# Kernel optimization log

Measured on AMD Instinct MI355X. Metric: run time of the kernel, lower is better.

Reference implementation:

```python
import jax, jax.numpy as jnp
import numpy as np

N = 100000
EPS = 1e-5

def gcn_conv(x, W, b, src, dst, n):
    # linear transform first (PyG GCNConv): [N, H]
    h = x @ W
    # add self-loops
    loop = jnp.arange(n, dtype=src.dtype)
    s = jnp.concatenate([src, loop])
    d = jnp.concatenate([dst, loop])
    # symmetric normalization deg^{-1/2}[s] * deg^{-1/2}[d]
    deg = jax.ops.segment_sum(jnp.ones_like(d, dtype=h.dtype), d, num_segments=n)
    dinv = jnp.where(deg > 0, jax.lax.rsqrt(jnp.maximum(deg, 1.0) * 0 + jnp.where(deg > 0, deg, 1.0)), 0.0)
    norm = dinv[s] * dinv[d]
    msg = h[s] * norm[:, None]          # gather + scale: [E+N, H]
    out = jax.ops.segment_sum(msg, d, num_segments=n)  # scatter-add
    return out + b

def batch_norm(x, gamma, beta):
    mu = jnp.mean(x, axis=0)
    var = jnp.mean((x - mu) ** 2, axis=0)  # biased var, as BatchNorm1d training
    return (x - mu) * jax.lax.rsqrt(var + EPS) * gamma + beta

def setup_inputs() -> dict:
    key = jax.random.key(0)
    ks = jax.random.split(key, 8)
    D, H, O = 64, 64, 32
    E = 1600000
    x = jax.random.normal(ks[0], (N, D), dtype=jnp.float32)
    edge_index = jax.random.randint(ks[1], (2, E), 0, N, dtype=jnp.int64)
    W1 = jax.random.normal(ks[2], (D, H), dtype=jnp.float32) / np.sqrt(D)
    b1 = jnp.zeros((H,), dtype=jnp.float32)
    W2 = jax.random.normal(ks[3], (H, H), dtype=jnp.float32) / np.sqrt(H)
    b2 = jnp.zeros((H,), dtype=jnp.float32)
    gamma1 = jnp.ones((H,), dtype=jnp.float32); beta1 = jnp.zeros((H,), dtype=jnp.float32)
    gamma2 = jnp.ones((H,), dtype=jnp.float32); beta2 = jnp.zeros((H,), dtype=jnp.float32)
    Wfc = jax.random.normal(ks[4], (H, O), dtype=jnp.float32) / np.sqrt(H)
    bfc = jnp.zeros((O,), dtype=jnp.float32)
    return {"x": x, "edge_index": edge_index, "W1": W1, "b1": b1, "gamma1": gamma1, "beta1": beta1,
            "W2": W2, "b2": b2, "gamma2": gamma2, "beta2": beta2, "Wfc": Wfc, "bfc": bfc}

def reference(x, edge_index, W1, b1, gamma1, beta1, W2, b2, gamma2, beta2, Wfc, bfc):
    src, dst = edge_index[0], edge_index[1]
    h = jax.nn.relu(gcn_conv(x, W1, b1, src, dst, N))
    h = batch_norm(h, gamma1, beta1)
    h = jax.nn.relu(gcn_conv(h, W2, b2, src, dst, N))
    h = batch_norm(h, gamma2, beta2)
    return h @ Wfc + bfc
```

## Files before the change

### kernel.cpp

```cpp
#include <hip/hip_runtime.h>
#include <hip/hip_bf16.h>
#include <cstdint>
#include <cstddef>

#define NS 8
#define SCHUNK 12500
#define BKB 512
#define SUBC 32

static __device__ __forceinline__ unsigned pack_bf16(float a, float b) {
  __hip_bfloat16 lo = __float2bfloat16(a), hi = __float2bfloat16(b);
  unsigned short ulo = *reinterpret_cast<unsigned short*>(&lo);
  unsigned short uhi = *reinterpret_cast<unsigned short*>(&hi);
  return ((unsigned)uhi << 16) | ulo;
}
static __device__ __forceinline__ float blo(unsigned u) {
  union { unsigned q; float f; } x; x.q = u << 16; return x.f;
}
static __device__ __forceinline__ float bhi(unsigned u) {
  union { unsigned q; float f; } x; x.q = u & 0xffff0000u; return x.f;
}


__launch_bounds__(256)
__global__ void bucket_kernel(const int* __restrict__ src, const int* __restrict__ dst,
                              int E, int cap, unsigned magic,
                              int* __restrict__ bcur,
                              int* __restrict__ bkt_d, int* __restrict__ bkt_s) {
  __shared__ int cnt8[NS], base8[NS], gbase8[NS], cur8[NS];
  __shared__ int stg_d[3200], stg_s[3200];
  int t = threadIdx.x;
  int chunk = (E + BKB - 1) / BKB;
  int ebeg = blockIdx.x * chunk;
  int eend = min(E, ebeg + chunk);
  int nloc = eend - ebeg;
  if (t < NS) { cnt8[t] = 0; cur8[t] = 0; }
  __syncthreads();

  int dl[13], sl[13]; unsigned cl[13];
  int nr = (nloc + 255) >> 8;
#pragma unroll 13
  for (int u = 0; u < nr; ++u) {
    int li = (u << 8) + t;
    bool v = li < nloc;
    int i = ebeg + (v ? li : 0);
    int d = v ? __builtin_nontemporal_load(&dst[i]) : 0;
    int s = v ? __builtin_nontemporal_load(&src[i]) : 0;
    unsigned sli = (unsigned)(((unsigned long long)(unsigned)d * magic) >> 45);
    dl[u] = d; sl[u] = s; cl[u] = sli;
    if (v) atomicAdd(&cnt8[sli], 1);
  }
  __syncthreads();
  if (t == 0) {
    int run = 0;
#pragma unroll
    for (int q = 0; q < NS; ++q) { base8[q] = run; run += cnt8[q]; }
  }
  __syncthreads();
  if (t < NS) gbase8[t] = atomicAdd(&bcur[t], cnt8[t]);
#pragma unroll 13
  for (int u = 0; u < nr; ++u) {
    int li = (u << 8) + t;
    if (li < nloc) {
      unsigned sli = cl[u];
      int pos = atomicAdd(&cur8[sli], 1) + base8[sli];
      stg_d[pos] = dl[u]; stg_s[pos] = sl[u];
    }
  }
  __syncthreads();
#pragma unroll
  for (int q = 0; q < NS; ++q) {
    int c = cnt8[q], b = base8[q], g = gbase8[q];
    int* od = bkt_d + (size_t)q * cap + g;
    int* os = bkt_s + (size_t)q * cap + g;
    for (int i = t; i < c; i += 256) { od[i] = stg_d[b + i]; os[i] = stg_s[b + i]; }
  }
}

__launch_bounds__(1024)
__global__ void count_b_kernel(const int* __restrict__ bkt_d, const int* __restrict__ bcur,
                               int cap, int n, int* __restrict__ partials) {
  __shared__ int hist[SCHUNK];
  int slice = blockIdx.x & (NS - 1), sub = blockIdx.x >> 3;
  int sbase = slice * SCHUNK;
  int bs = bcur[slice];
  const int* bk = bkt_d + (size_t)slice * cap;
  for (int l = threadIdx.x; l < SCHUNK; l += 1024) hist[l] = 0;
  __syncthreads();
  int beg = (int)((long long)sub * bs / SUBC);
  int end = (int)((long long)(sub + 1) * bs / SUBC);
  for (int i = beg + threadIdx.x; i < end; i += 1024)
    atomicAdd(&hist[bk[i] - sbase], 1);
  __syncthreads();
  for (int l = threadIdx.x; l < SCHUNK; l += 1024)
    partials[(size_t)sub * n + sbase + l] = hist[l];
}

__global__ void scan1_kernel(int* __restrict__ partials, int n, int* __restrict__ rowptr,
                             float* __restrict__ dinv, int* __restrict__ bsums) {
  __shared__ int sm[1024];
  int t = threadIdx.x;
  int gid = blockIdx.x * 1024 + t;
  int v = 0;
  if (gid < n) {
#pragma unroll
    for (int s = 0; s < SUBC; ++s) {
      int c = partials[(size_t)s * n + gid];
      partials[(size_t)s * n + gid] = v;
      v += c;
    }
    dinv[gid] = rsqrtf((float)(v + 1));
  }
  sm[t] = v;
  __syncthreads();
  for (int off = 1; off < 1024; off <<= 1) {
    int x = (t >= off) ? sm[t - off] : 0;
    __syncthreads();
    sm[t] += x;
    __syncthreads();
  }
  if (gid < n) rowptr[gid] = sm[t] - v;
  if (t == 1023) bsums[blockIdx.x] = sm[1023];
}

__global__ void scan2_kernel(int* __restrict__ bsums, int nb) {
  __shared__ int sm[1024];
  int t = threadIdx.x;
  int v = (t < nb) ? bsums[t] : 0;
  sm[t] = v;
  __syncthreads();
  for (int off = 1; off < 1024; off <<= 1) {
    int x = (t >= off) ? sm[t - off] : 0;
    __syncthreads();
    sm[t] += x;
    __syncthreads();
  }
  if (t < nb) bsums[t] = sm[t] - v;
}

__global__ void scan3_kernel(int n, int E, int* __restrict__ rowptr, const int* __restrict__ bsums) {
  int i = blockIdx.x * blockDim.x + threadIdx.x;
  if (i < n) rowptr[i] += bsums[i >> 10];
  if (i == 0) rowptr[n] = E;
}

__launch_bounds__(1024)
__global__ void scatter_b_kernel(const int* __restrict__ bkt_d, const int* __restrict__ bkt_s,
                                 const int* __restrict__ bcur, int cap, int n,
                                 const int* __restrict__ rowptr, const int* __restrict__ partials,
                                 int* __restrict__ adj) {
  __shared__ int base[SCHUNK];
  int slice = blockIdx.x & (NS - 1), sub = blockIdx.x >> 3;
  int sbase = slice * SCHUNK;
  int bs = bcur[slice];
  const int* bd = bkt_d + (size_t)slice * cap;
  const int* bsc = bkt_s + (size_t)slice * cap;
  const int* pref = partials + (size_t)sub * n;
  for (int l = threadIdx.x; l < SCHUNK; l += 1024)
    base[l] = rowptr[sbase + l] + pref[sbase + l];
  __syncthreads();
  int beg = (int)((long long)sub * bs / SUBC);
  int end = (int)((long long)(sub + 1) * bs / SUBC);
  for (int i = beg + threadIdx.x; i < end; i += 1024) {
    int d = bd[i], s = bsc[i];
    int pos = atomicAdd(&base[d - sbase], 1);
    adj[pos] = s;
  }
}


template <int OUT, bool BF16OUT, bool BN, bool ABF16>
__launch_bounds__(256)
__global__ void gemm_kernel(const void* __restrict__ Ap, const float* __restrict__ W,
                            const float* __restrict__ bnacc,
                            const float* __restrict__ gamma, const float* __restrict__ beta,
                            const float* __restrict__ bias, const float* __restrict__ rowscale,
                            void* __restrict__ Cout, int n, float invn) {
  constexpr int OQ = OUT / 4;
  __shared__ float lds[64 * 65];
  __shared__ float sc_s[64], sh_s[64];
  int t = threadIdx.x;
  int row0 = blockIdx.x * 64;
  int rows = n - row0; if (rows > 64) rows = 64;

  if (BN) {
    if (t < 64) {
      float su = 0.f, sq = 0.f;
#pragma unroll
      for (int c = 0; c < 8; ++c) {
        su += bnacc[c * 128 + t];
        sq += bnacc[c * 128 + 64 + t];
      }
      float mu = su * invn;
      float var = sq * invn - mu * mu;
      float sc = gamma[t] * rsqrtf(var + 1e-5f);
      sc_s[t] = sc;
      sh_s[t] = fmaf(-mu, sc, beta[t]);
    }
    __syncthreads();
  }

  if (ABF16) {
    const uint4* A4 = (const uint4*)((const unsigned short*)Ap + (size_t)row0 * 64);
#pragma unroll
    for (int j = 0; j < 2; ++j) {
      int idx = t + j * 256;
      int r = idx >> 3, c8 = idx & 7;
      uint4 v = make_uint4(0, 0, 0, 0);
      if (r < rows) v = A4[idx];
      float f[8] = {blo(v.x), bhi(v.x), blo(v.y), bhi(v.y),
                    blo(v.z), bhi(v.z), blo(v.w), bhi(v.w)};
      float* p = &lds[r * 65 + c8 * 8];
#pragma unroll
      for (int q = 0; q < 8; ++q) {
        float xv = f[q];
        if (BN) xv = fmaf(xv, sc_s[c8 * 8 + q], sh_s[c8 * 8 + q]);
        p[q] = xv;
      }
    }
  } else {
    const float4* A4 = (const float4*)((const float*)Ap + (size_t)row0 * 64);
#pragma unroll
    for (int j = 0; j < 4; ++j) {
      int idx = t + j * 256;
      int r = idx >> 4, c4 = idx & 15;
      float4 v = make_float4(0.f, 0.f, 0.f, 0.f);
      if (r < rows) v = A4[idx];
      if (BN) {
        int c = c4 * 4;
        v.x = fmaf(v.x, sc_s[c + 0], sh_s[c + 0]);
        v.y = fmaf(v.y, sc_s[c + 1], sh_s[c + 1]);
        v.z = fmaf(v.z, sc_s[c + 2], sh_s[c + 2]);
        v.w = fmaf(v.w, sc_s[c + 3], sh_s[c + 3]);
      }
      float* p = &lds[r * 65 + c4 * 4];
      p[0] = v.x; p[1] = v.y; p[2] = v.z; p[3] = v.w;
    }
  }
  __syncthreads();

  const int w = __builtin_amdgcn_readfirstlane(t >> 6);
  const int r = t & 63;
  float acc[OQ];
#pragma unroll
  for (int o = 0; o < OQ; ++o) acc[o] = 0.f;
  const float* Ar = &lds[r * 65];
  const float* Wp = W + w * OQ;
  for (int k = 0; k < 64; ++k) {
    float a = Ar[k];
#pragma unroll
    for (int o = 0; o < OQ; ++o) acc[o] = fmaf(a, Wp[k * OUT + o], acc[o]);
  }
  if (rowscale) {
    int rr = row0 + r; if (rr >= n) rr = n - 1;
    float rs = rowscale[rr];
#pragma unroll
    for (int o = 0; o < OQ; ++o) acc[o] *= rs;
  }
  if (bias) {
    const float* Bp = bias + w * OQ;
#pragma unroll
    for (int o = 0; o < OQ; ++o) acc[o] += Bp[o];
  }

  if (r < rows) {
    if (BF16OUT) {
      unsigned pk[OQ / 2];
#pragma unroll
      for (int o2 = 0; o2 < OQ / 2; ++o2) pk[o2] = pack_bf16(acc[2 * o2], acc[2 * o2 + 1]);
      uint4* cp = (uint4*)((__hip_bfloat16*)Cout + (size_t)(row0 + r) * OUT + w * OQ);
#pragma unroll
      for (int j = 0; j < OQ / 8; ++j) {
        uint4 v; v.x = pk[j * 4]; v.y = pk[j * 4 + 1]; v.z = pk[j * 4 + 2]; v.w = pk[j * 4 + 3];
        cp[j] = v;
      }
    } else {
      float4* cp = (float4*)((float*)Cout + (size_t)(row0 + r) * OUT + w * OQ);
#pragma unroll
      for (int j = 0; j < OQ / 4; ++j)
        cp[j] = make_float4(acc[j * 4], acc[j * 4 + 1], acc[j * 4 + 2], acc[j * 4 + 3]);
    }
  }
}


__launch_bounds__(256, 8)
__global__ void agg_kernel(const __hip_bfloat16* __restrict__ g, const int* __restrict__ rowptr,
                           const int* __restrict__ adj, const float* __restrict__ dinv,
                           const float* __restrict__ bias, __hip_bfloat16* __restrict__ out,
                           float* __restrict__ bnacc, int n) {
  const int tid = threadIdx.x;
  const int lane = tid & 63;
  const int wave = tid >> 6;
  const int grp = lane >> 3;
  const int sub = lane & 7;
  const int gw = blockIdx.x * 4 + wave;

  const unsigned short* gu = (const unsigned short*)g;

  int d = gw * 8 + grp;
  int beg = rowptr[d];
  int k = rowptr[d + 1] - beg;
  float di = dinv[d];

  const uint4 v0 = *(const uint4*)(gu + (((size_t)d) << 6) + sub * 8);
  float acc[8];
  acc[0] = blo(v0.x); acc[1] = bhi(v0.x);
  acc[2] = blo(v0.y); acc[3] = bhi(v0.y);
  acc[4] = blo(v0.z); acc[5] = bhi(v0.z);
  acc[6] = blo(v0.w); acc[7] = bhi(v0.w);

  int kmax = k;
  kmax = max(kmax, __shfl_xor(kmax, 8));
  kmax = max(kmax, __shfl_xor(kmax, 16));
  kmax = max(kmax, __shfl_xor(kmax, 32));

  for (int j0 = 0; j0 < kmax; j0 += 8) {
    uint4 vv[8];
    float w[8];
#pragma unroll
    for (int u = 0; u < 8; ++u) {
      int idx = j0 + u;
      int aoff = (idx < k) ? idx : 0;
      int s = __builtin_nontemporal_load(&adj[beg + aoff]);
      unsigned su = ((unsigned)s < (unsigned)n) ? (unsigned)s : (unsigned)d;
      vv[u] = *(const uint4*)(gu + (((size_t)su) << 6) + sub * 8);
      w[u] = (idx < k) ? 1.f : 0.f;
    }
#pragma unroll
    for (int u = 0; u < 8; ++u) {
      acc[0] = fmaf(w[u], blo(vv[u].x), acc[0]);
      acc[1] = fmaf(w[u], bhi(vv[u].x), acc[1]);
      acc[2] = fmaf(w[u], blo(vv[u].y), acc[2]);
      acc[3] = fmaf(w[u], bhi(vv[u].y), acc[3]);
      acc[4] = fmaf(w[u], blo(vv[u].z), acc[4]);
      acc[5] = fmaf(w[u], bhi(vv[u].z), acc[5]);
      acc[6] = fmaf(w[u], blo(vv[u].w), acc[6]);
      acc[7] = fmaf(w[u], bhi(vv[u].w), acc[7]);
    }
  }

  float bias8[8];
  {
    const float4* bp = (const float4*)(bias + sub * 8);
    float4 b0 = bp[0], b1 = bp[1];
    bias8[0]=b0.x; bias8[1]=b0.y; bias8[2]=b0.z; bias8[3]=b0.w;
    bias8[4]=b1.x; bias8[5]=b1.y; bias8[6]=b1.z; bias8[7]=b1.w;
  }

  float o[8], s1[8], s2[8];
#pragma unroll
  for (int j = 0; j < 8; ++j) {
    float v = fmaf(acc[j], di, bias8[j]);
    v = fmaxf(v, 0.f);
    o[j] = v;
    s1[j] = v;
    s2[j] = v * v;
  }
  uint4 ov;
  ov.x = pack_bf16(o[0], o[1]); ov.y = pack_bf16(o[2], o[3]);
  ov.z = pack_bf16(o[4], o[5]); ov.w = pack_bf16(o[6], o[7]);
  *(uint4*)((unsigned short*)out + (((size_t)d) << 6) + sub * 8) = ov;

#pragma unroll
  for (int j = 0; j < 8; ++j) {
    s1[j] += __shfl_xor(s1[j], 8);  s2[j] += __shfl_xor(s2[j], 8);
    s1[j] += __shfl_xor(s1[j], 16); s2[j] += __shfl_xor(s2[j], 16);
    s1[j] += __shfl_xor(s1[j], 32); s2[j] += __shfl_xor(s2[j], 32);
  }
  __shared__ float redA[4][64], redB[4][64];
  if (lane < 8) {
#pragma unroll
    for (int j = 0; j < 8; ++j) {
      redA[wave][sub * 8 + j] = s1[j];
      redB[wave][sub * 8 + j] = s2[j];
    }
  }
  __syncthreads();
  if (tid < 64) {
    float a = redA[0][tid] + redA[1][tid] + redA[2][tid] + redA[3][tid];
    float b = redB[0][tid] + redB[1][tid] + redB[2][tid] + redB[3][tid];
    float* dst = bnacc + (blockIdx.x & 7) * 128;
    atomicAdd(&dst[tid], a);
    atomicAdd(&dst[64 + tid], b);
  }
}


extern "C" void kernel_launch(void* const* d_in, const int* in_sizes, int n_in,
                              void* d_out, int out_size, void* d_ws, size_t ws_size,
                              hipStream_t stream) {
  const float* x      = (const float*)d_in[0];
  const int*   ei     = (const int*)d_in[1];
  const float* W1     = (const float*)d_in[2];
  const float* b1     = (const float*)d_in[3];
  const float* gamma1 = (const float*)d_in[4];
  const float* beta1  = (const float*)d_in[5];
  const float* W2     = (const float*)d_in[6];
  const float* b2     = (const float*)d_in[7];
  const float* gamma2 = (const float*)d_in[8];
  const float* beta2  = (const float*)d_in[9];
  const float* Wfc    = (const float*)d_in[10];
  const float* bfc    = (const float*)d_in[11];

  int n = in_sizes[0] / 64;
  int E = in_sizes[1] / 2;
  const int* src = ei;
  const int* dst = ei + E;

  char* base = (char*)d_ws;
  size_t off = 0;
  auto alloc = [&](size_t bytes) -> char* {
    char* p = base + off;
    off += (bytes + 255) & ~(size_t)255;
    return p;
  };
  int*   rowptr = (int*)alloc((size_t)(n + 1) * 4);
  int*   adj    = (int*)alloc(((size_t)E + 64) * 4);
  int*   bsums  = (int*)alloc(1024 * 4);
  float* dinv   = (float*)alloc((size_t)n * 4);
  float* bn     = (float*)alloc(2048 * 4);
  int*   bcur   = (int*)alloc(NS * 4);
  __hip_bfloat16* hbuf = (__hip_bfloat16*)alloc((size_t)n * 64 * 2);
  char*  rraw   = alloc((size_t)n * 64 * 4);
  __hip_bfloat16* rbuf = (__hip_bfloat16*)rraw;
  int cap = 210000;
  int* bkt_d = (int*)rraw;
  int* bkt_s = bkt_d + (size_t)NS * cap;
  int* partials = (int*)hbuf;
  (void)ws_size; (void)n_in; (void)out_size;

  hipMemsetAsync(bn, 0, 2048 * 4, stream);
  hipMemsetAsync(bcur, 0, NS * 4, stream);

  unsigned magic = (unsigned)(((1ULL << 45) + SCHUNK - 1) / SCHUNK);
  bucket_kernel<<<BKB, 256, 0, stream>>>(src, dst, E, cap, magic, bcur, bkt_d, bkt_s);
  count_b_kernel<<<NS * SUBC, 1024, 0, stream>>>(bkt_d, bcur, cap, n, partials);
  int nb = (n + 1023) / 1024;
  scan1_kernel<<<nb, 1024, 0, stream>>>(partials, n, rowptr, dinv, bsums);
  scan2_kernel<<<1, 1024, 0, stream>>>(bsums, nb);
  scan3_kernel<<<(n + 255) / 256, 256, 0, stream>>>(n, E, rowptr, bsums);
  scatter_b_kernel<<<NS * SUBC, 1024, 0, stream>>>(bkt_d, bkt_s, bcur, cap, n,
                                                   rowptr, partials, adj);

  int gg = (n + 63) / 64;
  int ga = n / 32;
  float invn = 1.0f / (float)n;
  gemm_kernel<64, true, false, false><<<gg, 256, 0, stream>>>(
      x, W1, nullptr, nullptr, nullptr, nullptr, dinv, hbuf, n, 0.f);
  agg_kernel<<<ga, 256, 0, stream>>>(hbuf, rowptr, adj, dinv, b1, rbuf, bn, n);
  gemm_kernel<64, true, true, true><<<gg, 256, 0, stream>>>(
      rbuf, W2, bn, gamma1, beta1, nullptr, dinv, hbuf, n, invn);
  agg_kernel<<<ga, 256, 0, stream>>>(hbuf, rowptr, adj, dinv, b2, rbuf, bn + 1024, n);
  gemm_kernel<32, false, true, true><<<gg, 256, 0, stream>>>(
      rbuf, Wfc, bn + 1024, gamma2, beta2, bfc, nullptr, d_out, n, invn);
}
```

Measured before the change: 271.6 us.

## Replace bucketed LDS CSR build with direct global atomic degree count and scatter

Replaces the multi-pass bucketing CSR construction (slice bucketing, per-slice shared-memory histograms, partial-count scans) with a direct global-atomic degree histogram and a global-atomic scatter into adjacency. This removes two passes over the bucket arrays and the 32-way partial prefix work. In exchange it relies on 1.6M global atomics per pass on random destinations, and the scatter writes to adj land at random addresses.

```diff
diff --git a/kernel.cpp b/kernel.cpp
--- a/kernel.cpp
+++ b/kernel.cpp
@@ -2,11 +2,6 @@
 #include <hip/hip_bf16.h>
 #include <cstdint>
 #include <cstddef>
-
-#define NS 8
-#define SCHUNK 12500
-#define BKB 512
-#define SUBC 32
 
 static __device__ __forceinline__ unsigned pack_bf16(float a, float b) {
   __hip_bfloat16 lo = __float2bfloat16(a), hi = __float2bfloat16(b);
@@ -23,92 +18,27 @@
 
 
 __launch_bounds__(256)
-__global__ void bucket_kernel(const int* __restrict__ src, const int* __restrict__ dst,
-                              int E, int cap, unsigned magic,
-                              int* __restrict__ bcur,
-                              int* __restrict__ bkt_d, int* __restrict__ bkt_s) {
-  __shared__ int cnt8[NS], base8[NS], gbase8[NS], cur8[NS];
-  __shared__ int stg_d[3200], stg_s[3200];
-  int t = threadIdx.x;
-  int chunk = (E + BKB - 1) / BKB;
-  int ebeg = blockIdx.x * chunk;
-  int eend = min(E, ebeg + chunk);
-  int nloc = eend - ebeg;
-  if (t < NS) { cnt8[t] = 0; cur8[t] = 0; }
-  __syncthreads();
-
-  int dl[13], sl[13]; unsigned cl[13];
-  int nr = (nloc + 255) >> 8;
-#pragma unroll 13
-  for (int u = 0; u < nr; ++u) {
-    int li = (u << 8) + t;
-    bool v = li < nloc;
-    int i = ebeg + (v ? li : 0);
-    int d = v ? __builtin_nontemporal_load(&dst[i]) : 0;
-    int s = v ? __builtin_nontemporal_load(&src[i]) : 0;
-    unsigned sli = (unsigned)(((unsigned long long)(unsigned)d * magic) >> 45);
-    dl[u] = d; sl[u] = s; cl[u] = sli;
-    if (v) atomicAdd(&cnt8[sli], 1);
-  }
-  __syncthreads();
-  if (t == 0) {
-    int run = 0;
-#pragma unroll
-    for (int q = 0; q < NS; ++q) { base8[q] = run; run += cnt8[q]; }
-  }
-  __syncthreads();
-  if (t < NS) gbase8[t] = atomicAdd(&bcur[t], cnt8[t]);
-#pragma unroll 13
-  for (int u = 0; u < nr; ++u) {
-    int li = (u << 8) + t;
-    if (li < nloc) {
-      unsigned sli = cl[u];
-      int pos = atomicAdd(&cur8[sli], 1) + base8[sli];
-      stg_d[pos] = dl[u]; stg_s[pos] = sl[u];
-    }
-  }
-  __syncthreads();
-#pragma unroll
-  for (int q = 0; q < NS; ++q) {
-    int c = cnt8[q], b = base8[q], g = gbase8[q];
-    int* od = bkt_d + (size_t)q * cap + g;
-    int* os = bkt_s + (size_t)q * cap + g;
-    for (int i = t; i < c; i += 256) { od[i] = stg_d[b + i]; os[i] = stg_s[b + i]; }
-  }
-}
-
-__launch_bounds__(1024)
-__global__ void count_b_kernel(const int* __restrict__ bkt_d, const int* __restrict__ bcur,
-                               int cap, int n, int* __restrict__ partials) {
-  __shared__ int hist[SCHUNK];
-  int slice = blockIdx.x & (NS - 1), sub = blockIdx.x >> 3;
-  int sbase = slice * SCHUNK;
-  int bs = bcur[slice];
-  const int* bk = bkt_d + (size_t)slice * cap;
-  for (int l = threadIdx.x; l < SCHUNK; l += 1024) hist[l] = 0;
-  __syncthreads();
-  int beg = (int)((long long)sub * bs / SUBC);
-  int end = (int)((long long)(sub + 1) * bs / SUBC);
-  for (int i = beg + threadIdx.x; i < end; i += 1024)
-    atomicAdd(&hist[bk[i] - sbase], 1);
-  __syncthreads();
-  for (int l = threadIdx.x; l < SCHUNK; l += 1024)
-    partials[(size_t)sub * n + sbase + l] = hist[l];
-}
-
-__global__ void scan1_kernel(int* __restrict__ partials, int n, int* __restrict__ rowptr,
+__global__ void deg_kernel(const int* __restrict__ dst, int E, int* __restrict__ deg) {
+  int i = (blockIdx.x * blockDim.x + threadIdx.x) * 4;
+  if (i + 3 < E) {
+    int4 d4 = *(const int4*)(dst + i);
+    atomicAdd(&deg[d4.x], 1);
+    atomicAdd(&deg[d4.y], 1);
+    atomicAdd(&deg[d4.z], 1);
+    atomicAdd(&deg[d4.w], 1);
+  } else {
+    for (int j = i; j < E; ++j) atomicAdd(&deg[dst[j]], 1);
+  }
+}
+
+__global__ void scan1_kernel(const int* __restrict__ deg, int n, int* __restrict__ rowptr,
                              float* __restrict__ dinv, int* __restrict__ bsums) {
   __shared__ int sm[1024];
   int t = threadIdx.x;
   int gid = blockIdx.x * 1024 + t;
   int v = 0;
   if (gid < n) {
-#pragma unroll
-    for (int s = 0; s < SUBC; ++s) {
-      int c = partials[(size_t)s * n + gid];
-      partials[(size_t)s * n + gid] = v;
-      v += c;
-    }
+    v = deg[gid];
     dinv[gid] = rsqrtf((float)(v + 1));
   }
   sm[t] = v;
@@ -138,33 +68,34 @@
   if (t < nb) bsums[t] = sm[t] - v;
 }
 
-__global__ void scan3_kernel(int n, int E, int* __restrict__ rowptr, const int* __restrict__ bsums) {
+__global__ void scan3_kernel(int n, int E, int* __restrict__ rowptr,
+                             const int* __restrict__ bsums, int* __restrict__ cur) {
   int i = blockIdx.x * blockDim.x + threadIdx.x;
-  if (i < n) rowptr[i] += bsums[i >> 10];
+  if (i < n) {
+    int v = rowptr[i] + bsums[i >> 10];
+    rowptr[i] = v;
+    cur[i] = v;
+  }
   if (i == 0) rowptr[n] = E;
 }
 
-__launch_bounds__(1024)
-__global__ void scatter_b_kernel(const int* __restrict__ bkt_d, const int* __restrict__ bkt_s,
-                                 const int* __restrict__ bcur, int cap, int n,
-                                 const int* __restrict__ rowptr, const int* __restrict__ partials,
-                                 int* __restrict__ adj) {
-  __shared__ int base[SCHUNK];
-  int slice = blockIdx.x & (NS - 1), sub = blockIdx.x >> 3;
-  int sbase = slice * SCHUNK;
-  int bs = bcur[slice];
-  const int* bd = bkt_d + (size_t)slice * cap;
-  const int* bsc = bkt_s + (size_t)slice * cap;
-  const int* pref = partials + (size_t)sub * n;
-  for (int l = threadIdx.x; l < SCHUNK; l += 1024)
-    base[l] = rowptr[sbase + l] + pref[sbase + l];
-  __syncthreads();
-  int beg = (int)((long long)sub * bs / SUBC);
-  int end = (int)((long long)(sub + 1) * bs / SUBC);
-  for (int i = beg + threadIdx.x; i < end; i += 1024) {
-    int d = bd[i], s = bsc[i];
-    int pos = atomicAdd(&base[d - sbase], 1);
-    adj[pos] = s;
+__launch_bounds__(256)
+__global__ void scat_kernel(const int* __restrict__ src, const int* __restrict__ dst, int E,
+                            int* __restrict__ cur, int* __restrict__ adj) {
+  int i = (blockIdx.x * blockDim.x + threadIdx.x) * 4;
+  if (i + 3 < E) {
+    int4 s4 = *(const int4*)(src + i);
+    int4 d4 = *(const int4*)(dst + i);
+    int p0 = atomicAdd(&cur[d4.x], 1);
+    int p1 = atomicAdd(&cur[d4.y], 1);
+    int p2 = atomicAdd(&cur[d4.z], 1);
+    int p3 = atomicAdd(&cur[d4.w], 1);
+    adj[p0] = s4.x; adj[p1] = s4.y; adj[p2] = s4.z; adj[p3] = s4.w;
+  } else {
+    for (int j = i; j < E; ++j) {
+      int p = atomicAdd(&cur[dst[j]], 1);
+      adj[p] = src[j];
+    }
   }
 }
 
@@ -420,28 +351,22 @@
   int*   bsums  = (int*)alloc(1024 * 4);
   float* dinv   = (float*)alloc((size_t)n * 4);
   float* bn     = (float*)alloc(2048 * 4);
-  int*   bcur   = (int*)alloc(NS * 4);
+  int*   deg    = (int*)alloc((size_t)n * 4);
+  int*   cur    = (int*)alloc((size_t)n * 4);
   __hip_bfloat16* hbuf = (__hip_bfloat16*)alloc((size_t)n * 64 * 2);
-  char*  rraw   = alloc((size_t)n * 64 * 4);
-  __hip_bfloat16* rbuf = (__hip_bfloat16*)rraw;
-  int cap = 210000;
-  int* bkt_d = (int*)rraw;
-  int* bkt_s = bkt_d + (size_t)NS * cap;
-  int* partials = (int*)hbuf;
+  __hip_bfloat16* rbuf = (__hip_bfloat16*)alloc((size_t)n * 64 * 2);
   (void)ws_size; (void)n_in; (void)out_size;
 
   hipMemsetAsync(bn, 0, 2048 * 4, stream);
-  hipMemsetAsync(bcur, 0, NS * 4, stream);
-
-  unsigned magic = (unsigned)(((1ULL << 45) + SCHUNK - 1) / SCHUNK);
-  bucket_kernel<<<BKB, 256, 0, stream>>>(src, dst, E, cap, magic, bcur, bkt_d, bkt_s);
-  count_b_kernel<<<NS * SUBC, 1024, 0, stream>>>(bkt_d, bcur, cap, n, partials);
+  hipMemsetAsync(deg, 0, (size_t)n * 4, stream);
+
+  int e4b = (E / 4 + 255) / 256;
+  deg_kernel<<<e4b, 256, 0, stream>>>(dst, E, deg);
   int nb = (n + 1023) / 1024;
-  scan1_kernel<<<nb, 1024, 0, stream>>>(partials, n, rowptr, dinv, bsums);
+  scan1_kernel<<<nb, 1024, 0, stream>>>(deg, n, rowptr, dinv, bsums);
   scan2_kernel<<<1, 1024, 0, stream>>>(bsums, nb);
-  scan3_kernel<<<(n + 255) / 256, 256, 0, stream>>>(n, E, rowptr, bsums);
-  scatter_b_kernel<<<NS * SUBC, 1024, 0, stream>>>(bkt_d, bkt_s, bcur, cap, n,
-                                                   rowptr, partials, adj);
+  scan3_kernel<<<(n + 255) / 256, 256, 0, stream>>>(n, E, rowptr, bsums, cur);
+  scat_kernel<<<e4b, 256, 0, stream>>>(src, dst, E, cur, adj);
 
   int gg = (n + 63) / 64;
   int ga = n / 32;
```

New measurement: 411.8 us. 1.52x slower.
